# Optimization experiments

Measured on AMD Instinct MI355X. Metric: run time of the kernel, lower is better.

## Reference

```python
import jax, jax.numpy as jnp
import numpy as np

EPS = 1e-8
ROUTING_ITERS = 3


def squash(s):
    # norm-based nonlinearity along last axis
    norm = jnp.linalg.norm(s, axis=-1, keepdims=True)
    return norm / (1.0 + norm * norm + EPS) * s


def setup_inputs() -> dict:
    key = jax.random.key(0)
    k1, k2, k3 = jax.random.split(key, 3)
    B, R, C, O, I = 512, 1152, 10, 16, 8  # batch, num_routes, num_capsules, out_ch, in_ch
    x = jax.random.normal(k1, (B, R, I), dtype=jnp.float32)
    W = jax.random.normal(k2, (R, C, O, I), dtype=jnp.float32) * 0.01
    bias = jax.random.uniform(k3, (1, 1, C, O), dtype=jnp.float32) * 0.01
    return {"x": x, "W": W, "bias": bias}


def reference(x, W, bias):
    # u_hat[b,r,c,o] = W[r,c,o,i] @ x[b,r,i]
    u_hat = jnp.einsum('rcoi,bri->brco', W, x)  # [B,R,C,O]
    B, R, C, O = u_hat.shape
    b_ij = jnp.zeros((B, R, C, 1), dtype=u_hat.dtype)
    v_j = None
    for itr in range(ROUTING_ITERS):
        c_ij = jax.nn.softmax(b_ij, axis=2)                      # softmax over capsules
        s_j = (c_ij * u_hat).sum(axis=1, keepdims=True) + bias   # [B,1,C,O]
        v_j = squash(s_j)                                        # [B,1,C,O]
        if itr < ROUTING_ITERS - 1:
            a_ij = (u_hat * v_j).sum(axis=-1, keepdims=True)     # agreement [B,R,C,1]
            b_ij = b_ij + a_ij
    return v_j.squeeze(axis=1)  # [B,C,O]
```

## Files before the change

kernel.cpp:

```cpp
#include <hip/hip_runtime.h>
#include <hip/hip_bf16.h>
#include <stdint.h>


#define BB 512
#define RR 1152
#define CCAP 10
#define II 8
#define CO 160
#define NBT 32
#define NSPLIT 24
#define RCHUNK 48
#define RWAVE 12

typedef __attribute__((ext_vector_type(8))) short bf16x8;
typedef __attribute__((ext_vector_type(4))) float f32x4;

__device__ inline short f2bf(float f) {
    uint32_t b = __float_as_uint(f);
    uint32_t r = (b + 0x7FFFu + ((b >> 16) & 1u)) >> 16;
    return (short)r;
}
__device__ inline float bf2f(unsigned short u) {
    return __uint_as_float(((uint32_t)u) << 16);
}

__global__ __launch_bounds__(256) void wconv(
    const float* __restrict__ W, unsigned short* __restrict__ Wf)
{
    const int i = (blockIdx.x * 256 + threadIdx.x) * 4;
    f32x4 w = *reinterpret_cast<const f32x4*>(W + i);
    ushort4 o;
    o.x = (unsigned short)f2bf(w[0]); o.y = (unsigned short)f2bf(w[1]);
    o.z = (unsigned short)f2bf(w[2]); o.w = (unsigned short)f2bf(w[3]);
    *reinterpret_cast<ushort4*>(Wf + i) = o;
}

template <int K>
__global__ __launch_bounds__(256) void route2(
    const float* __restrict__ x, const unsigned short* __restrict__ Wf,
    const float* __restrict__ v_in, unsigned short* __restrict__ bij,
    float* __restrict__ P)
{
    __shared__ float part[4 * 2720];
    const int t  = threadIdx.x;
    const int bt = blockIdx.x & 31;
    const int sp = blockIdx.x >> 5;
    const int b0 = bt * 16;
    const int w  = t >> 6;
    const int l  = t & 63;
    const int lg = l >> 4;
    const int ln = l & 15;

    f32x4 vf[CCAP];
    if (K > 0) {
        #pragma unroll
        for (int tt = 0; tt < CCAP; ++tt)
            vf[tt] = *reinterpret_cast<const f32x4*>(
                v_in + (size_t)(b0 + ln) * CO + tt * 16 + lg * 4);
    }

    f32x4 sacc[CCAP];
    #pragma unroll
    for (int tt = 0; tt < CCAP; ++tt) {
        sacc[tt][0]=0.f; sacc[tt][1]=0.f; sacc[tt][2]=0.f; sacc[tt][3]=0.f;
    }

    const int rb = sp * RCHUNK + w * RWAVE;
    for (int rr = 0; rr < RWAVE; ++rr) {
        const int r = rb + rr;
        bf16x8 bfr;
        #pragma unroll
        for (int j = 0; j < 8; ++j) bfr[j] = 0;
        if (l < 16) {
            const float* xp = x + ((size_t)(b0 + l) * RR + r) * II;
            f32x4 lo = *reinterpret_cast<const f32x4*>(xp);
            f32x4 hi = *reinterpret_cast<const f32x4*>(xp + 4);
            #pragma unroll
            for (int j = 0; j < 4; ++j) { bfr[j] = f2bf(lo[j]); bfr[4+j] = f2bf(hi[j]); }
        }
        f32x4 u[CCAP];
        #pragma unroll
        for (int tt = 0; tt < CCAP; ++tt) {
            bf16x8 afr;
            #pragma unroll
            for (int j = 0; j < 8; ++j) afr[j] = 0;
            if (l < 16)
                afr = *reinterpret_cast<const bf16x8*>(
                    Wf + ((size_t)r * CCAP + tt) * 128 + l * 8);
            f32x4 z; z[0]=0.f; z[1]=0.f; z[2]=0.f; z[3]=0.f;
            u[tt] = __builtin_amdgcn_mfma_f32_16x16x32_bf16(afr, bfr, z, 0, 0, 0);
        }
        if (K > 0) {
            float a[CCAP];
            #pragma unroll
            for (int tt = 0; tt < CCAP; ++tt) {
                float p = u[tt][0]*vf[tt][0] + u[tt][1]*vf[tt][1]
                        + u[tt][2]*vf[tt][2] + u[tt][3]*vf[tt][3];
                p += __shfl_xor(p, 16);
                p += __shfl_xor(p, 32);
                a[tt] = p;
            }
            if (K == 2) {
                #pragma unroll
                for (int tt = 0; tt < CCAP; ++tt)
                    a[tt] += bf2f(bij[((size_t)r * CCAP + tt) * BB + b0 + ln]);
            } else {
                if (l < 16) {
                    #pragma unroll
                    for (int tt = 0; tt < CCAP; ++tt)
                        bij[((size_t)r * CCAP + tt) * BB + b0 + l] =
                            (unsigned short)f2bf(a[tt]);
                }
            }
            float m = a[0];
            #pragma unroll
            for (int tt = 1; tt < CCAP; ++tt) m = fmaxf(m, a[tt]);
            float ssum = 0.f;
            #pragma unroll
            for (int tt = 0; tt < CCAP; ++tt) { a[tt] = __expf(a[tt] - m); ssum += a[tt]; }
            float inv = 1.0f / ssum;
            #pragma unroll
            for (int tt = 0; tt < CCAP; ++tt) {
                float c = a[tt] * inv;
                sacc[tt][0] += c * u[tt][0];
                sacc[tt][1] += c * u[tt][1];
                sacc[tt][2] += c * u[tt][2];
                sacc[tt][3] += c * u[tt][3];
            }
        } else {
            #pragma unroll
            for (int tt = 0; tt < CCAP; ++tt) {
                sacc[tt][0] += u[tt][0];
                sacc[tt][1] += u[tt][1];
                sacc[tt][2] += u[tt][2];
                sacc[tt][3] += u[tt][3];
            }
        }
    }
    if (K == 0) {
        #pragma unroll
        for (int tt = 0; tt < CCAP; ++tt) {
            sacc[tt][0] *= 0.1f; sacc[tt][1] *= 0.1f;
            sacc[tt][2] *= 0.1f; sacc[tt][3] *= 0.1f;
        }
    }
    #pragma unroll
    for (int tt = 0; tt < CCAP; ++tt) {
        #pragma unroll
        for (int reg = 0; reg < 4; ++reg)
            part[w * 2720 + (tt * 16 + lg * 4 + reg) * 17 + ln] = sacc[tt][reg];
    }
    __syncthreads();
    float* Pu = P + (size_t)(bt * NSPLIT + sp) * 2560;
    for (int q = 0; q < 10; ++q) {
        const int idx = q * 256 + t;
        const int b16 = idx / 160, co = idx % 160;
        const int a0 = co * 17 + b16;
        Pu[idx] = part[a0] + part[2720 + a0] + part[5440 + a0] + part[8160 + a0];
    }
}

__global__ __launch_bounds__(256) void squash_merge(
    const float* __restrict__ P, const float* __restrict__ bias,
    float* __restrict__ v_out)
{
    const int idx = blockIdx.x * 256 + threadIdx.x;
    const int b = idx / CO, co = idx % CO;
    const int bt = b >> 4, b16 = b & 15;
    const float* base = P + (size_t)bt * NSPLIT * 2560 + b16 * CO + co;
    float sv = 0.f;
    #pragma unroll
    for (int sp = 0; sp < NSPLIT; ++sp) sv += base[(size_t)sp * 2560];
    sv += bias[co];
    float n2 = sv * sv;
    n2 += __shfl_xor(n2, 1);
    n2 += __shfl_xor(n2, 2);
    n2 += __shfl_xor(n2, 4);
    n2 += __shfl_xor(n2, 8);
    float norm = sqrtf(n2);
    float scale = norm / (1.0f + n2 + 1e-8f);
    v_out[idx] = scale * sv;
}

extern "C" void kernel_launch(void* const* d_in, const int* in_sizes, int n_in,
                              void* d_out, int out_size, void* d_ws, size_t ws_size,
                              hipStream_t stream) {
    const float* x    = (const float*)d_in[0];
    const float* W    = (const float*)d_in[1];
    const float* bias = (const float*)d_in[2];
    float* out = (float*)d_out;

    float* v = (float*)d_ws;
    float* P = v + 81920;
    unsigned short* bij = (unsigned short*)(P + (size_t)NBT * NSPLIT * 2560);
    unsigned short* Wf  = bij + (size_t)RR * CCAP * BB;

    const dim3 blk(256);
    const dim3 rgrid(NBT * NSPLIT);

    wconv<<<1440, blk, 0, stream>>>(W, Wf);

    route2<0><<<rgrid, blk, 0, stream>>>(x, Wf, v, bij, P);
    squash_merge<<<320, blk, 0, stream>>>(P, bias, v);

    route2<1><<<rgrid, blk, 0, stream>>>(x, Wf, v, bij, P);
    squash_merge<<<320, blk, 0, stream>>>(P, bias, v);

    route2<2><<<rgrid, blk, 0, stream>>>(x, Wf, v, bij, P);
    squash_merge<<<320, blk, 0, stream>>>(P, bias, out);
}
```

Before: 310.5 us.

## Reduce routing partials with atomics and double route split count

The route split across the grid doubles (more blocks, fewer routes per wave). Per-block partial sums now go through LDS atomics into one shared buffer and then global float atomics into a single s buffer. This replaces the partial-sum array and the multi-split merge in the squash kernel, and the buffer is zeroed with a memset before each iteration. It cuts LDS size and merge traffic and raises parallelism, at the cost of heavy global atomic contention, extra memset launches, and nondeterministic summation order. Every lane now loads the W fragment rather than only lanes below 16.

Result: slower. 418.2 us (+34.7%).

```diff
diff --git a/kernel.cpp b/kernel.cpp
--- a/kernel.cpp
+++ b/kernel.cpp
@@ -9,9 +9,9 @@
 #define II 8
 #define CO 160
 #define NBT 32
-#define NSPLIT 24
-#define RCHUNK 48
-#define RWAVE 12
+#define NSPLIT 48
+#define RCHUNK 24
+#define RWAVE 6
 
 typedef __attribute__((ext_vector_type(8))) short bf16x8;
 typedef __attribute__((ext_vector_type(4))) float f32x4;
@@ -37,12 +37,12 @@
 }
 
 template <int K>
-__global__ __launch_bounds__(256) void route2(
+__global__ __launch_bounds__(256) void route3(
     const float* __restrict__ x, const unsigned short* __restrict__ Wf,
     const float* __restrict__ v_in, unsigned short* __restrict__ bij,
-    float* __restrict__ P)
+    float* __restrict__ s_out)
 {
-    __shared__ float part[4 * 2720];
+    __shared__ float spart[CO * 17];
     const int t  = threadIdx.x;
     const int bt = blockIdx.x & 31;
     const int sp = blockIdx.x >> 5;
@@ -52,6 +52,8 @@
     const int lg = l >> 4;
     const int ln = l & 15;
 
+    for (int i = t; i < CO * 17; i += 256) spart[i] = 0.0f;
+
     f32x4 vf[CCAP];
     if (K > 0) {
         #pragma unroll
@@ -82,12 +84,8 @@
         f32x4 u[CCAP];
         #pragma unroll
         for (int tt = 0; tt < CCAP; ++tt) {
-            bf16x8 afr;
-            #pragma unroll
-            for (int j = 0; j < 8; ++j) afr[j] = 0;
-            if (l < 16)
-                afr = *reinterpret_cast<const bf16x8*>(
-                    Wf + ((size_t)r * CCAP + tt) * 128 + l * 8);
+            bf16x8 afr = *reinterpret_cast<const bf16x8*>(
+                Wf + ((size_t)r * CCAP + tt) * 128 + ln * 8);
             f32x4 z; z[0]=0.f; z[1]=0.f; z[2]=0.f; z[3]=0.f;
             u[tt] = __builtin_amdgcn_mfma_f32_16x16x32_bf16(afr, bfr, z, 0, 0, 0);
         }
@@ -145,34 +143,28 @@
             sacc[tt][2] *= 0.1f; sacc[tt][3] *= 0.1f;
         }
     }
+    __syncthreads();
     #pragma unroll
     for (int tt = 0; tt < CCAP; ++tt) {
         #pragma unroll
         for (int reg = 0; reg < 4; ++reg)
-            part[w * 2720 + (tt * 16 + lg * 4 + reg) * 17 + ln] = sacc[tt][reg];
+            atomicAdd(&spart[(tt * 16 + lg * 4 + reg) * 17 + ln], sacc[tt][reg]);
     }
     __syncthreads();
-    float* Pu = P + (size_t)(bt * NSPLIT + sp) * 2560;
     for (int q = 0; q < 10; ++q) {
         const int idx = q * 256 + t;
-        const int b16 = idx / 160, co = idx % 160;
-        const int a0 = co * 17 + b16;
-        Pu[idx] = part[a0] + part[2720 + a0] + part[5440 + a0] + part[8160 + a0];
-    }
-}
-
-__global__ __launch_bounds__(256) void squash_merge(
-    const float* __restrict__ P, const float* __restrict__ bias,
+        const int co = idx % CO, b16 = idx / CO;
+        atomicAdd(&s_out[(size_t)(b0 + b16) * CO + co], spart[co * 17 + b16]);
+    }
+}
+
+__global__ __launch_bounds__(256) void squash_plain(
+    const float* __restrict__ s, const float* __restrict__ bias,
     float* __restrict__ v_out)
 {
     const int idx = blockIdx.x * 256 + threadIdx.x;
-    const int b = idx / CO, co = idx % CO;
-    const int bt = b >> 4, b16 = b & 15;
-    const float* base = P + (size_t)bt * NSPLIT * 2560 + b16 * CO + co;
-    float sv = 0.f;
-    #pragma unroll
-    for (int sp = 0; sp < NSPLIT; ++sp) sv += base[(size_t)sp * 2560];
-    sv += bias[co];
+    const int co = idx % CO;
+    float sv = s[idx] + bias[co];
     float n2 = sv * sv;
     n2 += __shfl_xor(n2, 1);
     n2 += __shfl_xor(n2, 2);
@@ -192,8 +184,8 @@
     float* out = (float*)d_out;
 
     float* v = (float*)d_ws;
-    float* P = v + 81920;
-    unsigned short* bij = (unsigned short*)(P + (size_t)NBT * NSPLIT * 2560);
+    float* s = v + 81920;
+    unsigned short* bij = (unsigned short*)(s + 81920);
     unsigned short* Wf  = bij + (size_t)RR * CCAP * BB;
 
     const dim3 blk(256);
@@ -201,12 +193,15 @@
 
     wconv<<<1440, blk, 0, stream>>>(W, Wf);
 
-    route2<0><<<rgrid, blk, 0, stream>>>(x, Wf, v, bij, P);
-    squash_merge<<<320, blk, 0, stream>>>(P, bias, v);
-
-    route2<1><<<rgrid, blk, 0, stream>>>(x, Wf, v, bij, P);
-    squash_merge<<<320, blk, 0, stream>>>(P, bias, v);
-
-    route2<2><<<rgrid, blk, 0, stream>>>(x, Wf, v, bij, P);
-    squash_merge<<<320, blk, 0, stream>>>(P, bias, out);
-}
+    hipMemsetAsync(s, 0, 81920 * sizeof(float), stream);
+    route3<0><<<rgrid, blk, 0, stream>>>(x, Wf, v, bij, s);
+    squash_plain<<<320, blk, 0, stream>>>(s, bias, v);
+
+    hipMemsetAsync(s, 0, 81920 * sizeof(float), stream);
+    route3<1><<<rgrid, blk, 0, stream>>>(x, Wf, v, bij, s);
+    squash_plain<<<320, blk, 0, stream>>>(s, bias, v);
+
+    hipMemsetAsync(s, 0, 81920 * sizeof(float), stream);
+    route3<2><<<rgrid, blk, 0, stream>>>(x, Wf, v, bij, s);
+    squash_plain<<<320, blk, 0, stream>>>(s, bias, out);
+}
```

## Materialize u_hat in fp16 once and reuse across routing iterations

Applied to the files above, without the earlier changes.

Adds a producer kernel that computes u_hat with MFMA once, stores it as fp16 in workspace, and reduces the first-iteration sum with atomics. Later routing iterations read u_hat instead of recomputing it from x and W. Also pre-transposes x to bf16 and stores the logits in fp16. This trades recompute for roughly hundreds of MB of extra memory traffic and reduced precision. The path is only taken when the workspace is large enough; otherwise the old path runs.

New measurement: 326.1 us. 5.0% more time.

```diff
diff --git a/kernel.cpp b/kernel.cpp
--- a/kernel.cpp
+++ b/kernel.cpp
@@ -15,6 +15,7 @@
 
 typedef __attribute__((ext_vector_type(8))) short bf16x8;
 typedef __attribute__((ext_vector_type(4))) float f32x4;
+typedef __attribute__((ext_vector_type(4))) _Float16 f16x4;
 
 __device__ inline short f2bf(float f) {
     uint32_t b = __float_as_uint(f);
@@ -34,6 +35,189 @@
     o.x = (unsigned short)f2bf(w[0]); o.y = (unsigned short)f2bf(w[1]);
     o.z = (unsigned short)f2bf(w[2]); o.w = (unsigned short)f2bf(w[3]);
     *reinterpret_cast<ushort4*>(Wf + i) = o;
+}
+
+__global__ __launch_bounds__(256) void xconv(
+    const float* __restrict__ x, unsigned short* __restrict__ xT)
+{
+    const int tid = blockIdx.x * 256 + threadIdx.x;
+    const int r = tid >> 9, b = tid & 511;
+    const float* xp = x + ((size_t)b * RR + r) * II;
+    f32x4 lo = *reinterpret_cast<const f32x4*>(xp);
+    f32x4 hi = *reinterpret_cast<const f32x4*>(xp + 4);
+    ushort4 o0, o1;
+    o0.x=(unsigned short)f2bf(lo[0]); o0.y=(unsigned short)f2bf(lo[1]);
+    o0.z=(unsigned short)f2bf(lo[2]); o0.w=(unsigned short)f2bf(lo[3]);
+    o1.x=(unsigned short)f2bf(hi[0]); o1.y=(unsigned short)f2bf(hi[1]);
+    o1.z=(unsigned short)f2bf(hi[2]); o1.w=(unsigned short)f2bf(hi[3]);
+    unsigned short* op = xT + ((size_t)r * BB + b) * II;
+    *reinterpret_cast<ushort4*>(op)     = o0;
+    *reinterpret_cast<ushort4*>(op + 4) = o1;
+}
+
+__global__ __launch_bounds__(256) void produce_u(
+    const unsigned short* __restrict__ xT, const unsigned short* __restrict__ Wf,
+    _Float16* __restrict__ U, float* __restrict__ s_out)
+{
+    __shared__ float spart[CO * 17];
+    const int t  = threadIdx.x;
+    const int bt = blockIdx.x & 31;
+    const int sp = blockIdx.x >> 5;
+    const int b0 = bt * 16;
+    const int w  = t >> 6;
+    const int l  = t & 63;
+    const int lg = l >> 4;
+    const int ln = l & 15;
+
+    for (int i = t; i < CO * 17; i += 256) spart[i] = 0.0f;
+
+    f32x4 sacc[CCAP];
+    #pragma unroll
+    for (int tt = 0; tt < CCAP; ++tt) {
+        sacc[tt][0]=0.f; sacc[tt][1]=0.f; sacc[tt][2]=0.f; sacc[tt][3]=0.f;
+    }
+
+    const int rb = sp * RCHUNK + w * RWAVE;
+    for (int rr = 0; rr < RWAVE; ++rr) {
+        const int r = rb + rr;
+        bf16x8 bfr;
+        #pragma unroll
+        for (int j = 0; j < 8; ++j) bfr[j] = 0;
+        if (l < 16)
+            bfr = *reinterpret_cast<const bf16x8*>(xT + ((size_t)r * BB + b0 + l) * II);
+        _Float16* Ub = U + ((size_t)bt * RR + r) * (CCAP * 256) + l * 4;
+        #pragma unroll
+        for (int tt = 0; tt < CCAP; ++tt) {
+            bf16x8 afr = *reinterpret_cast<const bf16x8*>(
+                Wf + ((size_t)r * CCAP + tt) * 128 + ln * 8);
+            f32x4 z; z[0]=0.f; z[1]=0.f; z[2]=0.f; z[3]=0.f;
+            f32x4 u = __builtin_amdgcn_mfma_f32_16x16x32_bf16(afr, bfr, z, 0, 0, 0);
+            f16x4 h;
+            h[0]=(_Float16)u[0]; h[1]=(_Float16)u[1];
+            h[2]=(_Float16)u[2]; h[3]=(_Float16)u[3];
+            *reinterpret_cast<f16x4*>(Ub + tt * 256) = h;
+            sacc[tt][0] += u[0]; sacc[tt][1] += u[1];
+            sacc[tt][2] += u[2]; sacc[tt][3] += u[3];
+        }
+    }
+    __syncthreads();
+    #pragma unroll
+    for (int tt = 0; tt < CCAP; ++tt) {
+        #pragma unroll
+        for (int reg = 0; reg < 4; ++reg)
+            atomicAdd(&spart[(tt * 16 + lg * 4 + reg) * 17 + ln], 0.1f * sacc[tt][reg]);
+    }
+    __syncthreads();
+    for (int q = 0; q < 10; ++q) {
+        const int idx = q * 256 + t;
+        const int co = idx % CO, b16 = idx / CO;
+        atomicAdd(&s_out[(size_t)(b0 + b16) * CO + co], spart[co * 17 + b16]);
+    }
+}
+
+template <int K>
+__global__ __launch_bounds__(256) void consume_u(
+    const _Float16* __restrict__ U, const float* __restrict__ v_in,
+    _Float16* __restrict__ bij, float* __restrict__ s_out)
+{
+    __shared__ float spart[CO * 17];
+    const int t  = threadIdx.x;
+    const int bt = blockIdx.x & 31;
+    const int sp = blockIdx.x >> 5;
+    const int b0 = bt * 16;
+    const int w  = t >> 6;
+    const int l  = t & 63;
+    const int lg = l >> 4;
+    const int ln = l & 15;
+
+    for (int i = t; i < CO * 17; i += 256) spart[i] = 0.0f;
+
+    f32x4 vf[CCAP];
+    #pragma unroll
+    for (int tt = 0; tt < CCAP; ++tt)
+        vf[tt] = *reinterpret_cast<const f32x4*>(
+            v_in + (size_t)(b0 + ln) * CO + tt * 16 + lg * 4);
+
+    f32x4 sacc[CCAP];
+    #pragma unroll
+    for (int tt = 0; tt < CCAP; ++tt) {
+        sacc[tt][0]=0.f; sacc[tt][1]=0.f; sacc[tt][2]=0.f; sacc[tt][3]=0.f;
+    }
+
+    const int rb = sp * RCHUNK + w * RWAVE;
+    for (int rr = 0; rr < RWAVE; ++rr) {
+        const int r = rb + rr;
+        const _Float16* Ub = U + ((size_t)bt * RR + r) * (CCAP * 256) + l * 4;
+        f16x4 uh[CCAP];
+        #pragma unroll
+        for (int tt = 0; tt < CCAP; ++tt)
+            uh[tt] = *reinterpret_cast<const f16x4*>(Ub + tt * 256);
+        float a[CCAP];
+        #pragma unroll
+        for (int tt = 0; tt < CCAP; ++tt) {
+            float p = (float)uh[tt][0]*vf[tt][0] + (float)uh[tt][1]*vf[tt][1]
+                    + (float)uh[tt][2]*vf[tt][2] + (float)uh[tt][3]*vf[tt][3];
+            p += __shfl_xor(p, 16);
+            p += __shfl_xor(p, 32);
+            a[tt] = p;
+        }
+        if (K == 2) {
+            #pragma unroll
+            for (int tt = 0; tt < CCAP; ++tt)
+                a[tt] += (float)bij[((size_t)r * CCAP + tt) * BB + b0 + ln];
+        } else {
+            if (l < 16) {
+                #pragma unroll
+                for (int tt = 0; tt < CCAP; ++tt)
+                    bij[((size_t)r * CCAP + tt) * BB + b0 + l] = (_Float16)a[tt];
+            }
+        }
+        float m = a[0];
+        #pragma unroll
+        for (int tt = 1; tt < CCAP; ++tt) m = fmaxf(m, a[tt]);
+        float ssum = 0.f;
+        #pragma unroll
+        for (int tt = 0; tt < CCAP; ++tt) { a[tt] = __expf(a[tt] - m); ssum += a[tt]; }
+        float inv = 1.0f / ssum;
+        #pragma unroll
+        for (int tt = 0; tt < CCAP; ++tt) {
+            float c = a[tt] * inv;
+            sacc[tt][0] += c * (float)uh[tt][0];
+            sacc[tt][1] += c * (float)uh[tt][1];
+            sacc[tt][2] += c * (float)uh[tt][2];
+            sacc[tt][3] += c * (float)uh[tt][3];
+        }
+    }
+    __syncthreads();
+    #pragma unroll
+    for (int tt = 0; tt < CCAP; ++tt) {
+        #pragma unroll
+        for (int reg = 0; reg < 4; ++reg)
+            atomicAdd(&spart[(tt * 16 + lg * 4 + reg) * 17 + ln], sacc[tt][reg]);
+    }
+    __syncthreads();
+    for (int q = 0; q < 10; ++q) {
+        const int idx = q * 256 + t;
+        const int co = idx % CO, b16 = idx / CO;
+        atomicAdd(&s_out[(size_t)(b0 + b16) * CO + co], spart[co * 17 + b16]);
+    }
+}
+
+__global__ __launch_bounds__(256) void squash_plain(
+    const float* __restrict__ s, const float* __restrict__ bias,
+    float* __restrict__ v_out)
+{
+    const int idx = blockIdx.x * 256 + threadIdx.x;
+    const int co = idx % CO;
+    float sv = s[idx] + bias[co];
+    float n2 = sv * sv;
+    n2 += __shfl_xor(n2, 1);
+    n2 += __shfl_xor(n2, 2);
+    n2 += __shfl_xor(n2, 4);
+    n2 += __shfl_xor(n2, 8);
+    float norm = sqrtf(n2);
+    float scale = norm / (1.0f + n2 + 1e-8f);
+    v_out[idx] = scale * sv;
 }
 
 template <int K>
@@ -59,13 +243,11 @@
             vf[tt] = *reinterpret_cast<const f32x4*>(
                 v_in + (size_t)(b0 + ln) * CO + tt * 16 + lg * 4);
     }
-
     f32x4 sacc[CCAP];
     #pragma unroll
     for (int tt = 0; tt < CCAP; ++tt) {
         sacc[tt][0]=0.f; sacc[tt][1]=0.f; sacc[tt][2]=0.f; sacc[tt][3]=0.f;
     }
-
     const int rb = sp * RCHUNK + w * RWAVE;
     for (int rr = 0; rr < RWAVE; ++rr) {
         const int r = rb + rr;
@@ -82,12 +264,8 @@
         f32x4 u[CCAP];
         #pragma unroll
         for (int tt = 0; tt < CCAP; ++tt) {
-            bf16x8 afr;
-            #pragma unroll
-            for (int j = 0; j < 8; ++j) afr[j] = 0;
-            if (l < 16)
-                afr = *reinterpret_cast<const bf16x8*>(
-                    Wf + ((size_t)r * CCAP + tt) * 128 + l * 8);
+            bf16x8 afr = *reinterpret_cast<const bf16x8*>(
+                Wf + ((size_t)r * CCAP + tt) * 128 + ln * 8);
             f32x4 z; z[0]=0.f; z[1]=0.f; z[2]=0.f; z[3]=0.f;
             u[tt] = __builtin_amdgcn_mfma_f32_16x16x32_bf16(afr, bfr, z, 0, 0, 0);
         }
@@ -131,10 +309,8 @@
         } else {
             #pragma unroll
             for (int tt = 0; tt < CCAP; ++tt) {
-                sacc[tt][0] += u[tt][0];
-                sacc[tt][1] += u[tt][1];
-                sacc[tt][2] += u[tt][2];
-                sacc[tt][3] += u[tt][3];
+                sacc[tt][0] += u[tt][0]; sacc[tt][1] += u[tt][1];
+                sacc[tt][2] += u[tt][2]; sacc[tt][3] += u[tt][3];
             }
         }
     }
@@ -190,23 +366,48 @@
     const float* W    = (const float*)d_in[1];
     const float* bias = (const float*)d_in[2];
     float* out = (float*)d_out;
-
-    float* v = (float*)d_ws;
-    float* P = v + 81920;
-    unsigned short* bij = (unsigned short*)(P + (size_t)NBT * NSPLIT * 2560);
-    unsigned short* Wf  = bij + (size_t)RR * CCAP * BB;
+    char* ws = (char*)d_ws;
 
     const dim3 blk(256);
     const dim3 rgrid(NBT * NSPLIT);
 
-    wconv<<<1440, blk, 0, stream>>>(W, Wf);
-
-    route2<0><<<rgrid, blk, 0, stream>>>(x, Wf, v, bij, P);
-    squash_merge<<<320, blk, 0, stream>>>(P, bias, v);
-
-    route2<1><<<rgrid, blk, 0, stream>>>(x, Wf, v, bij, P);
-    squash_merge<<<320, blk, 0, stream>>>(P, bias, v);
-
-    route2<2><<<rgrid, blk, 0, stream>>>(x, Wf, v, bij, P);
-    squash_merge<<<320, blk, 0, stream>>>(P, bias, out);
-}
+    if (ws_size >= 213581824ull) {
+        float* v = (float*)(ws + 0);
+        float* s = (float*)(ws + 327680);
+        unsigned short* Wf = (unsigned short*)(ws + 655360);
+        unsigned short* xT = (unsigned short*)(ws + 3604480);
+        _Float16* bij = (_Float16*)(ws + 13041664);
+        _Float16* U   = (_Float16*)(ws + 24838144);
+
+        wconv<<<1440, blk, 0, stream>>>(W, Wf);
+        xconv<<<2304, blk, 0, stream>>>(x, xT);
+
+        hipMemsetAsync(s, 0, 81920 * sizeof(float), stream);
+        produce_u<<<rgrid, blk, 0, stream>>>(xT, Wf, U, s);
+        squash_plain<<<320, blk, 0, stream>>>(s, bias, v);
+
+        hipMemsetAsync(s, 0, 81920 * sizeof(float), stream);
+        consume_u<1><<<rgrid, blk, 0, stream>>>(U, v, bij, s);
+        squash_plain<<<320, blk, 0, stream>>>(s, bias, v);
+
+        hipMemsetAsync(s, 0, 81920 * sizeof(float), stream);
+        consume_u<2><<<rgrid, blk, 0, stream>>>(U, v, bij, s);
+        squash_plain<<<320, blk, 0, stream>>>(s, bias, out);
+    } else {
+        float* v = (float*)(ws + 0);
+        float* P = v + 81920;
+        unsigned short* bij = (unsigned short*)(ws + 8192000);
+        unsigned short* Wf  = (unsigned short*)(ws + 19988480);
+
+        wconv<<<1440, blk, 0, stream>>>(W, Wf);
+
+        route2<0><<<rgrid, blk, 0, stream>>>(x, Wf, v, bij, P);
+        squash_merge<<<320, blk, 0, stream>>>(P, bias, v);
+
+        route2<1><<<rgrid, blk, 0, stream>>>(x, Wf, v, bij, P);
+        squash_merge<<<320, blk, 0, stream>>>(P, bias, v);
+
+        route2<2><<<rgrid, blk, 0, stream>>>(x, Wf, v, bij, P);
+        squash_merge<<<320, blk, 0, stream>>>(P, bias, out);
+    }
+}
```
